# Kernel optimization log

Measured on AMD Instinct MI355X. Metric: run time of the kernel, lower is better.

The kernel has to match this reference:

```python
import jax, jax.numpy as jnp
import numpy as np


def setup_inputs() -> dict:
    key = jax.random.key(0)
    k1, k2, k3, k4, k5 = jax.random.split(key, 5)
    B, Te, Td, H = 16, 256, 128, 512
    return {
        "encoder_out_seq": jax.random.normal(k1, (B, Te, H), dtype=jnp.float32),
        "decoder_out_seq": jax.random.normal(k2, (B, Td, H), dtype=jnp.float32),
        "W_a": jax.random.normal(k3, (H, H), dtype=jnp.float32) * 0.02,
        "U_a": jax.random.normal(k4, (H, H), dtype=jnp.float32) * 0.02,
        "V_a": jax.random.normal(k5, (H, 1), dtype=jnp.float32) * 0.02,
    }


def reference(encoder_out_seq, decoder_out_seq, W_a, U_a, V_a):
    # encoder_out_seq: [B, Te, H], decoder_out_seq: [B, Td, H]
    # Original loops over decoder timesteps via K.rnn; the math per step is
    # independent, so we compute all timesteps at once (same result).
    W_s = jnp.einsum("beh,hk->bek", encoder_out_seq, W_a)      # [B, Te, H]
    U_h = jnp.einsum("bdh,hk->bdk", decoder_out_seq, U_a)      # [B, Td, H]
    # energies: tanh(W_s + U_h) @ V_a -> [B, Td, Te]
    act = jnp.tanh(W_s[:, None, :, :] + U_h[:, :, None, :])     # [B, Td, Te, H]
    e = jnp.einsum("bdeh,h->bde", act, V_a[:, 0])               # [B, Td, Te]
    e = jax.nn.softmax(e, axis=-1)                              # softmax over encoder steps
    # context: sum_e e * enc -> [B, Td, H]
    c = jnp.einsum("bde,beh->bdh", e, encoder_out_seq)
    return (c, e)
```

## Files before the change

kernel.cpp:

```cpp
#include <hip/hip_runtime.h>

#define B_  16
#define TE_ 256
#define TD_ 128
#define H_  512

#define C_TANH 2.88539008177792681472f
#define LOG2E  1.44269504088896340736f

typedef __attribute__((ext_vector_type(8))) short short8v;
typedef __attribute__((ext_vector_type(4))) float floatx4;

__device__ __forceinline__ float wave_sum(float v) {
#pragma unroll
  for (int m = 32; m; m >>= 1) v += __shfl_xor(v, m, 64);
  return v;
}
__device__ __forceinline__ float wave_max(float v) {
#pragma unroll
  for (int m = 32; m; m >>= 1) v = fmaxf(v, __shfl_xor(v, m, 64));
  return v;
}
__device__ __forceinline__ ushort f2bf(float f) {
  unsigned u = __builtin_bit_cast(unsigned, f);
  u += 0x7fffu + ((u >> 16) & 1u);
  return (ushort)(u >> 16);
}
__device__ __forceinline__ float bf2f(ushort u) {
  return __builtin_bit_cast(float, (unsigned)u << 16);
}
__device__ __forceinline__ unsigned pk2(float a, float b) {
  return (unsigned)f2bf(a) | ((unsigned)f2bf(b) << 16);
}

__global__ __launch_bounds__(256) void prep_T(
    const float* __restrict__ enc, const float* __restrict__ Wa,
    const float* __restrict__ Ua, ushort* __restrict__ encT,
    ushort* __restrict__ WaT, ushort* __restrict__ UaT)
{
  __shared__ float tl[32 * 66];
  const int tid = threadIdx.x;
  const int x = blockIdx.x, y = blockIdx.y, z = blockIdx.z;
  const int r = tid >> 3, g = tid & 7;
  const int hh = tid >> 2, tq = tid & 3;

  const float* s;
  ushort* d;
  long dstr;
  int r0, c0;
  if (y < 8) {
    s = enc + (size_t)z * TE_ * H_;
    d = encT + (size_t)z * H_ * TE_;
    dstr = TE_;
    r0 = y * 32; c0 = x * 64;
  } else {
    s = (y == 8) ? Wa : Ua;
    d = (y == 8) ? WaT : UaT;
    dstr = H_;
    r0 = z * 32; c0 = x * 64;
  }

  float4 f0 = *(const float4*)(s + (size_t)(r0 + r) * H_ + c0 + g * 8);
  float4 f1 = *(const float4*)(s + (size_t)(r0 + r) * H_ + c0 + g * 8 + 4);
  float* t = &tl[r * 66 + g * 8];
  t[0] = f0.x; t[1] = f0.y; t[2] = f0.z; t[3] = f0.w;
  t[4] = f1.x; t[5] = f1.y; t[6] = f1.z; t[7] = f1.w;
  __syncthreads();
  float v[8];
#pragma unroll
  for (int i = 0; i < 8; ++i) v[i] = tl[(tq * 8 + i) * 66 + hh];
  uint4 tp = {pk2(v[0], v[1]), pk2(v[2], v[3]), pk2(v[4], v[5]), pk2(v[6], v[7])};
  *(uint4*)(d + (size_t)(c0 + hh) * dstr + r0 + tq * 8) = tp;
}

template <bool CVTA, bool CVTB>
__device__ __forceinline__ void gemm_core(
    const void* Asrc, const void* Bsrc, long lda, long ldb, int K,
    int arow0, int brow0, ushort* As, ushort* Bs, floatx4* acc)
{
  const int tid = threadIdx.x;
  const int l = tid & 63, w = tid >> 6;
  const int l15 = l & 15, l4 = l >> 4;
  const int srow = tid >> 3, kg = tid & 7;
  const int ks = kg >> 2, kc = (kg & 3) << 3;
  const int dsA = ks * 2560 + kc;

  const float*  Af = (const float*)Asrc;
  const ushort* Ab = (const ushort*)Asrc;
  const float*  Bf = (const float*)Bsrc;
  const ushort* Bb = (const ushort*)Bsrc;

  const long aoff0 = (long)(arow0 + srow) * lda + kg * 8;
  const long aoff1 = (long)(arow0 + 32 + srow) * lda + kg * 8;
  const long boff0 = (long)(brow0 + srow) * ldb + kg * 8;
  const long boff1 = (long)(brow0 + 32 + srow) * ldb + kg * 8;

  short8v a0r, a1r, b0r, b1r;
  float4 fa00, fa01, fa10, fa11, fb00, fb01, fb10, fb11;

  auto LD = [&](int kt) {
    if constexpr (CVTA) {
      fa00 = *(const float4*)(Af + aoff0 + kt);
      fa01 = *(const float4*)(Af + aoff0 + kt + 4);
      fa10 = *(const float4*)(Af + aoff1 + kt);
      fa11 = *(const float4*)(Af + aoff1 + kt + 4);
    } else {
      a0r = *(const short8v*)(Ab + aoff0 + kt);
      a1r = *(const short8v*)(Ab + aoff1 + kt);
    }
    if constexpr (CVTB) {
      fb00 = *(const float4*)(Bf + boff0 + kt);
      fb01 = *(const float4*)(Bf + boff0 + kt + 4);
      fb10 = *(const float4*)(Bf + boff1 + kt);
      fb11 = *(const float4*)(Bf + boff1 + kt + 4);
    } else {
      b0r = *(const short8v*)(Bb + boff0 + kt);
      b1r = *(const short8v*)(Bb + boff1 + kt);
    }
  };
  auto ST = [&]() {
    if constexpr (CVTA) {
      uint4 p0 = {pk2(fa00.x, fa00.y), pk2(fa00.z, fa00.w),
                  pk2(fa01.x, fa01.y), pk2(fa01.z, fa01.w)};
      uint4 p1 = {pk2(fa10.x, fa10.y), pk2(fa10.z, fa10.w),
                  pk2(fa11.x, fa11.y), pk2(fa11.z, fa11.w)};
      *(uint4*)&As[dsA + srow * 40] = p0;
      *(uint4*)&As[dsA + (32 + srow) * 40] = p1;
    } else {
      *(short8v*)&As[dsA + srow * 40] = a0r;
      *(short8v*)&As[dsA + (32 + srow) * 40] = a1r;
    }
    if constexpr (CVTB) {
      uint4 p0 = {pk2(fb00.x, fb00.y), pk2(fb00.z, fb00.w),
                  pk2(fb01.x, fb01.y), pk2(fb01.z, fb01.w)};
      uint4 p1 = {pk2(fb10.x, fb10.y), pk2(fb10.z, fb10.w),
                  pk2(fb11.x, fb11.y), pk2(fb11.z, fb11.w)};
      *(uint4*)&Bs[dsA + srow * 40] = p0;
      *(uint4*)&Bs[dsA + (32 + srow) * 40] = p1;
    } else {
      *(short8v*)&Bs[dsA + srow * 40] = b0r;
      *(short8v*)&Bs[dsA + (32 + srow) * 40] = b1r;
    }
  };

  LD(0);
  for (int kt = 0; kt < K; kt += 64) {
    if (kt) __syncthreads();
    ST();
    __syncthreads();
    if (kt + 64 < K) LD(kt + 64);
#pragma unroll
    for (int kk = 0; kk < 2; ++kk) {
      short8v av = *(short8v*)&As[kk * 2560 + (w * 16 + l15) * 40 + l4 * 8];
#pragma unroll
      for (int nt = 0; nt < 4; ++nt) {
        short8v bv = *(short8v*)&Bs[kk * 2560 + (nt * 16 + l15) * 40 + l4 * 8];
        acc[nt] = __builtin_amdgcn_mfma_f32_16x16x32_bf16(av, bv, acc[nt], 0, 0, 0);
      }
    }
  }
}

__global__ __launch_bounds__(256) void gemm_phaseA(
    const float* __restrict__ enc, const ushort* __restrict__ WaT,
    ushort* __restrict__ E_T,
    const float* __restrict__ dec, const ushort* __restrict__ UaT,
    float* __restrict__ eU)
{
  __shared__ __attribute__((aligned(16))) ushort As[5120];
  __shared__ __attribute__((aligned(16))) ushort Bs[5120];

  const int tid = threadIdx.x;
  const int l = tid & 63, w = tid >> 6;
  const int l15 = l & 15, l4 = l >> 4;
  const int id = blockIdx.x;

  floatx4 acc[4] = {};

  if (id < 512) {
    const int x = id & 7, k = id >> 3;
    const int bm = k >> 3;
    const int bn = x * 8 + (k & 7);
    gemm_core<false, true>(WaT, enc, H_, H_, H_, bm * 64, bn * 64, As, Bs, acc);
    const int bb = bn >> 2, t0 = (bn & 3) * 64;
    const int hb = bm * 64 + w * 16 + (l4 << 2);
#pragma unroll
    for (int nt = 0; nt < 4; ++nt) {
      const int t = t0 + nt * 16 + l15;
#pragma unroll
      for (int r = 0; r < 4; ++r)
        E_T[((size_t)bb * H_ + hb + r) * TE_ + t] =
            f2bf(__builtin_amdgcn_exp2f(C_TANH * acc[nt][r]));
    }
  } else {
    const int i2 = id - 512;
    const int x = i2 & 7, k = i2 >> 3;
    const int bm = x * 4 + (k & 3);
    const int bn = k >> 2;
    gemm_core<true, false>(dec, UaT, H_, H_, H_, bm * 64, bn * 64, As, Bs, acc);
    const int growb = bm * 64 + w * 16 + (l4 << 2);
#pragma unroll
    for (int nt = 0; nt < 4; ++nt) {
      const int gcol = bn * 64 + nt * 16 + l15;
#pragma unroll
      for (int r = 0; r < 4; ++r)
        eU[(size_t)(growb + r) * H_ + gcol] =
            __builtin_amdgcn_exp2f(C_TANH * acc[nt][r]);
    }
  }
}

__global__ __launch_bounds__(256) void gemm_ctx(
    const ushort* __restrict__ eB, const ushort* __restrict__ encT,
    float* __restrict__ C)
{
  __shared__ __attribute__((aligned(16))) ushort As[5120];
  __shared__ __attribute__((aligned(16))) ushort Bs[5120];

  const int tid = threadIdx.x;
  const int l = tid & 63, w = tid >> 6;
  const int l15 = l & 15, l4 = l >> 4;
  const long z = blockIdx.z;
  const int bm = blockIdx.y, bn = blockIdx.x;

  floatx4 acc[4] = {};
  gemm_core<false, false>(eB + z * TD_ * TE_, encT + z * (long)H_ * TE_,
                          TE_, TE_, TE_, bm * 64, bn * 64, As, Bs, acc);

  const int growb = bm * 64 + w * 16 + (l4 << 2);
#pragma unroll
  for (int nt = 0; nt < 4; ++nt) {
    const int gcol = bn * 64 + nt * 16 + l15;
#pragma unroll
    for (int r = 0; r < 4; ++r)
      C[(z * TD_ + growb + r) * (long)H_ + gcol] = acc[nt][r];
  }
}

__global__ __launch_bounds__(512) void energies_softmax(
    const ushort* __restrict__ E_T, const float* __restrict__ eU,
    const float* __restrict__ Va, float* __restrict__ e_out,
    ushort* __restrict__ eB)
{
  __shared__ float part[2][8][TE_];

  const int tid  = threadIdx.x;
  const int lane = tid & 63;
  const int wv   = __builtin_amdgcn_readfirstlane(tid >> 6);
  const int id   = blockIdx.x;
  const int xcd  = id & 7, j = id >> 3;
  const int b    = (xcd << 1) | (j >> 6);
  const int d0   = (j & 63) << 1;

  float4 v0 = *(const float4*)(Va + (lane << 2));
  float4 v1 = *(const float4*)(Va + 256 + (lane << 2));
  const float svtot =
      wave_sum(v0.x + v0.y + v0.z + v0.w + v1.x + v1.y + v1.z + v1.w);

  const float* u0 = eU + (size_t)(b * TD_ + d0 + 0) * H_ + wv * 64;
  const float* u1 = eU + (size_t)(b * TD_ + d0 + 1) * H_ + wv * 64;
  const float* vp = Va + wv * 64;
  const ushort* ep = E_T + ((size_t)(b * H_) + wv * 64) * TE_ + (lane << 2);

  float p0[4] = {}, p1[4] = {};

#pragma unroll 4
  for (int h = 0; h < 64; ++h) {
    const float sV = vp[h];
    const float sU0 = u0[h], sU1 = u1[h];
    ushort4 ew = *(const ushort4*)(ep + (size_t)h * TE_);
    float e0 = bf2f(ew.x), e1 = bf2f(ew.y), e2 = bf2f(ew.z), e3 = bf2f(ew.w);
    p0[0] = fmaf(sV, __builtin_amdgcn_rcpf(fmaf(e0, sU0, 1.f)), p0[0]);
    p0[1] = fmaf(sV, __builtin_amdgcn_rcpf(fmaf(e1, sU0, 1.f)), p0[1]);
    p0[2] = fmaf(sV, __builtin_amdgcn_rcpf(fmaf(e2, sU0, 1.f)), p0[2]);
    p0[3] = fmaf(sV, __builtin_amdgcn_rcpf(fmaf(e3, sU0, 1.f)), p0[3]);
    p1[0] = fmaf(sV, __builtin_amdgcn_rcpf(fmaf(e0, sU1, 1.f)), p1[0]);
    p1[1] = fmaf(sV, __builtin_amdgcn_rcpf(fmaf(e1, sU1, 1.f)), p1[1]);
    p1[2] = fmaf(sV, __builtin_amdgcn_rcpf(fmaf(e2, sU1, 1.f)), p1[2]);
    p1[3] = fmaf(sV, __builtin_amdgcn_rcpf(fmaf(e3, sU1, 1.f)), p1[3]);
  }

  *(float4*)&part[0][wv][lane << 2] = *(float4*)p0;
  *(float4*)&part[1][wv][lane << 2] = *(float4*)p1;
  __syncthreads();

  if (wv < 2) {
    float l4v[4] = {0.f, 0.f, 0.f, 0.f};
#pragma unroll
    for (int w = 0; w < 8; ++w) {
      float4 q = *(const float4*)&part[wv][w][lane << 2];
      l4v[0] += q.x; l4v[1] += q.y; l4v[2] += q.z; l4v[3] += q.w;
    }
#pragma unroll
    for (int q = 0; q < 4; ++q) l4v[q] = svtot - 2.f * l4v[q];
    float m = wave_max(fmaxf(fmaxf(l4v[0], l4v[1]), fmaxf(l4v[2], l4v[3])));
    float p[4];
    float s = 0.f;
#pragma unroll
    for (int q = 0; q < 4; ++q) {
      p[q] = __builtin_amdgcn_exp2f((l4v[q] - m) * LOG2E);
      s += p[q];
    }
    s = wave_sum(s);
    const float inv = 1.0f / s;
    float4 ov = {p[0] * inv, p[1] * inv, p[2] * inv, p[3] * inv};
    const size_t ro = (size_t)(b * TD_ + d0 + wv) * TE_ + (lane << 2);
    *(float4*)(e_out + ro) = ov;
    ushort4 ob = {f2bf(ov.x), f2bf(ov.y), f2bf(ov.z), f2bf(ov.w)};
    *(ushort4*)(eB + ro) = ob;
  }
}

extern "C" void kernel_launch(void* const* d_in, const int* in_sizes, int n_in,
                              void* d_out, int out_size, void* d_ws, size_t ws_size,
                              hipStream_t stream) {
  const float* enc = (const float*)d_in[0];
  const float* dec = (const float*)d_in[1];
  const float* Wa  = (const float*)d_in[2];
  const float* Ua  = (const float*)d_in[3];
  const float* Va  = (const float*)d_in[4];

  float* out_c = (float*)d_out;
  float* out_e = out_c + (size_t)B_ * TD_ * H_;

  char* w8 = (char*)d_ws;
  ushort* E_T  = (ushort*)(w8);
  float*  eU   = (float*)(w8 + (4u << 20));
  ushort* WaT  = (ushort*)(w8 + (8u << 20));
  ushort* UaT  = (ushort*)(w8 + (8u << 20) + (512u << 10));
  ushort* encT = (ushort*)(w8 + (9u << 20));
  ushort* eB   = (ushort*)(w8 + (13u << 20));

  prep_T<<<dim3(8, 10, 16), 256, 0, stream>>>(enc, Wa, Ua, encT, WaT, UaT);

  gemm_phaseA<<<768, 256, 0, stream>>>(enc, WaT, E_T, dec, UaT, eU);

  energies_softmax<<<1024, 512, 0, stream>>>(E_T, eU, Va, out_e, eB);

  gemm_ctx<<<dim3(8, 2, 16), 256, 0, stream>>>(eB, encT, out_c);
}
```

Measured before the change: 58.65 us.

## Remove transpose prep kernel by transposing fp32 operands inside GEMM tile loads

Drops the separate prep_T kernel that transposed and converted enc, W_a and U_a to bf16. The GEMM core gains a third load mode that reads row-major fp32 K-major tiles and transposes them into shared memory while packing to bf16. This removes one kernel launch and a full read and write pass over enc and the weights. In exchange each GEMM does scalar 32-bit LDS stores, which may cause bank conflicts, and re-reads fp32 data, doubling global traffic for those operands.

Result: no change. 58.52 us (-0.2%).

```diff
diff --git a/kernel.cpp b/kernel.cpp
--- a/kernel.cpp
+++ b/kernel.cpp
@@ -33,47 +33,7 @@
   return (unsigned)f2bf(a) | ((unsigned)f2bf(b) << 16);
 }
 
-__global__ __launch_bounds__(256) void prep_T(
-    const float* __restrict__ enc, const float* __restrict__ Wa,
-    const float* __restrict__ Ua, ushort* __restrict__ encT,
-    ushort* __restrict__ WaT, ushort* __restrict__ UaT)
-{
-  __shared__ float tl[32 * 66];
-  const int tid = threadIdx.x;
-  const int x = blockIdx.x, y = blockIdx.y, z = blockIdx.z;
-  const int r = tid >> 3, g = tid & 7;
-  const int hh = tid >> 2, tq = tid & 3;
-
-  const float* s;
-  ushort* d;
-  long dstr;
-  int r0, c0;
-  if (y < 8) {
-    s = enc + (size_t)z * TE_ * H_;
-    d = encT + (size_t)z * H_ * TE_;
-    dstr = TE_;
-    r0 = y * 32; c0 = x * 64;
-  } else {
-    s = (y == 8) ? Wa : Ua;
-    d = (y == 8) ? WaT : UaT;
-    dstr = H_;
-    r0 = z * 32; c0 = x * 64;
-  }
-
-  float4 f0 = *(const float4*)(s + (size_t)(r0 + r) * H_ + c0 + g * 8);
-  float4 f1 = *(const float4*)(s + (size_t)(r0 + r) * H_ + c0 + g * 8 + 4);
-  float* t = &tl[r * 66 + g * 8];
-  t[0] = f0.x; t[1] = f0.y; t[2] = f0.z; t[3] = f0.w;
-  t[4] = f1.x; t[5] = f1.y; t[6] = f1.z; t[7] = f1.w;
-  __syncthreads();
-  float v[8];
-#pragma unroll
-  for (int i = 0; i < 8; ++i) v[i] = tl[(tq * 8 + i) * 66 + hh];
-  uint4 tp = {pk2(v[0], v[1]), pk2(v[2], v[3]), pk2(v[4], v[5]), pk2(v[6], v[7])};
-  *(uint4*)(d + (size_t)(c0 + hh) * dstr + r0 + tq * 8) = tp;
-}
-
-template <bool CVTA, bool CVTB>
+template <int MA, int MB>
 __device__ __forceinline__ void gemm_core(
     const void* Asrc, const void* Bsrc, long lda, long ldb, int K,
     int arow0, int brow0, ushort* As, ushort* Bs, floatx4* acc)
@@ -82,8 +42,9 @@
   const int l = tid & 63, w = tid >> 6;
   const int l15 = l & 15, l4 = l >> 4;
   const int srow = tid >> 3, kg = tid & 7;
-  const int ks = kg >> 2, kc = (kg & 3) << 3;
-  const int dsA = ks * 2560 + kc;
+  const int dsRC = (kg >> 2) * 2560 + ((kg & 3) << 3);
+  const int kp = tid >> 3, hg = tid & 7;
+  const int dsT = (kp >> 4) * 2560 + ((kp << 1) & 31);
 
   const float*  Af = (const float*)Asrc;
   const ushort* Ab = (const ushort*)Asrc;
@@ -96,50 +57,82 @@
   const long boff1 = (long)(brow0 + 32 + srow) * ldb + kg * 8;
 
   short8v a0r, a1r, b0r, b1r;
-  float4 fa00, fa01, fa10, fa11, fb00, fb01, fb10, fb11;
+  float4 fa0, fa1, fa2, fa3, fb0, fb1, fb2, fb3;
 
   auto LD = [&](int kt) {
-    if constexpr (CVTA) {
-      fa00 = *(const float4*)(Af + aoff0 + kt);
-      fa01 = *(const float4*)(Af + aoff0 + kt + 4);
-      fa10 = *(const float4*)(Af + aoff1 + kt);
-      fa11 = *(const float4*)(Af + aoff1 + kt + 4);
-    } else {
+    if constexpr (MA == 0) {
       a0r = *(const short8v*)(Ab + aoff0 + kt);
       a1r = *(const short8v*)(Ab + aoff1 + kt);
-    }
-    if constexpr (CVTB) {
-      fb00 = *(const float4*)(Bf + boff0 + kt);
-      fb01 = *(const float4*)(Bf + boff0 + kt + 4);
-      fb10 = *(const float4*)(Bf + boff1 + kt);
-      fb11 = *(const float4*)(Bf + boff1 + kt + 4);
+    } else if constexpr (MA == 1) {
+      fa0 = *(const float4*)(Af + aoff0 + kt);
+      fa1 = *(const float4*)(Af + aoff0 + kt + 4);
+      fa2 = *(const float4*)(Af + aoff1 + kt);
+      fa3 = *(const float4*)(Af + aoff1 + kt + 4);
     } else {
+      const long base = (long)(kt + 2 * kp) * lda + arow0 + hg * 8;
+      fa0 = *(const float4*)(Af + base);
+      fa1 = *(const float4*)(Af + base + 4);
+      fa2 = *(const float4*)(Af + base + lda);
+      fa3 = *(const float4*)(Af + base + lda + 4);
+    }
+    if constexpr (MB == 0) {
       b0r = *(const short8v*)(Bb + boff0 + kt);
       b1r = *(const short8v*)(Bb + boff1 + kt);
+    } else if constexpr (MB == 1) {
+      fb0 = *(const float4*)(Bf + boff0 + kt);
+      fb1 = *(const float4*)(Bf + boff0 + kt + 4);
+      fb2 = *(const float4*)(Bf + boff1 + kt);
+      fb3 = *(const float4*)(Bf + boff1 + kt + 4);
+    } else {
+      const long base = (long)(kt + 2 * kp) * ldb + brow0 + hg * 8;
+      fb0 = *(const float4*)(Bf + base);
+      fb1 = *(const float4*)(Bf + base + 4);
+      fb2 = *(const float4*)(Bf + base + ldb);
+      fb3 = *(const float4*)(Bf + base + ldb + 4);
     }
   };
   auto ST = [&]() {
-    if constexpr (CVTA) {
-      uint4 p0 = {pk2(fa00.x, fa00.y), pk2(fa00.z, fa00.w),
-                  pk2(fa01.x, fa01.y), pk2(fa01.z, fa01.w)};
-      uint4 p1 = {pk2(fa10.x, fa10.y), pk2(fa10.z, fa10.w),
-                  pk2(fa11.x, fa11.y), pk2(fa11.z, fa11.w)};
-      *(uint4*)&As[dsA + srow * 40] = p0;
-      *(uint4*)&As[dsA + (32 + srow) * 40] = p1;
+    if constexpr (MA == 0) {
+      *(short8v*)&As[dsRC + srow * 40] = a0r;
+      *(short8v*)&As[dsRC + (32 + srow) * 40] = a1r;
+    } else if constexpr (MA == 1) {
+      uint4 p0 = {pk2(fa0.x, fa0.y), pk2(fa0.z, fa0.w),
+                  pk2(fa1.x, fa1.y), pk2(fa1.z, fa1.w)};
+      uint4 p1 = {pk2(fa2.x, fa2.y), pk2(fa2.z, fa2.w),
+                  pk2(fa3.x, fa3.y), pk2(fa3.z, fa3.w)};
+      *(uint4*)&As[dsRC + srow * 40] = p0;
+      *(uint4*)&As[dsRC + (32 + srow) * 40] = p1;
     } else {
-      *(short8v*)&As[dsA + srow * 40] = a0r;
-      *(short8v*)&As[dsA + (32 + srow) * 40] = a1r;
-    }
-    if constexpr (CVTB) {
-      uint4 p0 = {pk2(fb00.x, fb00.y), pk2(fb00.z, fb00.w),
-                  pk2(fb01.x, fb01.y), pk2(fb01.z, fb01.w)};
-      uint4 p1 = {pk2(fb10.x, fb10.y), pk2(fb10.z, fb10.w),
-                  pk2(fb11.x, fb11.y), pk2(fb11.z, fb11.w)};
-      *(uint4*)&Bs[dsA + srow * 40] = p0;
-      *(uint4*)&Bs[dsA + (32 + srow) * 40] = p1;
+      const int h0 = hg * 8;
+      *(unsigned*)&As[dsT + (h0 + 0) * 40] = pk2(fa0.x, fa2.x);
+      *(unsigned*)&As[dsT + (h0 + 1) * 40] = pk2(fa0.y, fa2.y);
+      *(unsigned*)&As[dsT + (h0 + 2) * 40] = pk2(fa0.z, fa2.z);
+      *(unsigned*)&As[dsT + (h0 + 3) * 40] = pk2(fa0.w, fa2.w);
+      *(unsigned*)&As[dsT + (h0 + 4) * 40] = pk2(fa1.x, fa3.x);
+      *(unsigned*)&As[dsT + (h0 + 5) * 40] = pk2(fa1.y, fa3.y);
+      *(unsigned*)&As[dsT + (h0 + 6) * 40] = pk2(fa1.z, fa3.z);
+      *(unsigned*)&As[dsT + (h0 + 7) * 40] = pk2(fa1.w, fa3.w);
+    }
+    if constexpr (MB == 0) {
+      *(short8v*)&Bs[dsRC + srow * 40] = b0r;
+      *(short8v*)&Bs[dsRC + (32 + srow) * 40] = b1r;
+    } else if constexpr (MB == 1) {
+      uint4 p0 = {pk2(fb0.x, fb0.y), pk2(fb0.z, fb0.w),
+                  pk2(fb1.x, fb1.y), pk2(fb1.z, fb1.w)};
+      uint4 p1 = {pk2(fb2.x, fb2.y), pk2(fb2.z, fb2.w),
+                  pk2(fb3.x, fb3.y), pk2(fb3.z, fb3.w)};
+      *(uint4*)&Bs[dsRC + srow * 40] = p0;
+      *(uint4*)&Bs[dsRC + (32 + srow) * 40] = p1;
     } else {
-      *(short8v*)&Bs[dsA + srow * 40] = b0r;
-      *(short8v*)&Bs[dsA + (32 + srow) * 40] = b1r;
+      const int h0 = hg * 8;
+      *(unsigned*)&Bs[dsT + (h0 + 0) * 40] = pk2(fb0.x, fb2.x);
+      *(unsigned*)&Bs[dsT + (h0 + 1) * 40] = pk2(fb0.y, fb2.y);
+      *(unsigned*)&Bs[dsT + (h0 + 2) * 40] = pk2(fb0.z, fb2.z);
+      *(unsigned*)&Bs[dsT + (h0 + 3) * 40] = pk2(fb0.w, fb2.w);
+      *(unsigned*)&Bs[dsT + (h0 + 4) * 40] = pk2(fb1.x, fb3.x);
+      *(unsigned*)&Bs[dsT + (h0 + 5) * 40] = pk2(fb1.y, fb3.y);
+      *(unsigned*)&Bs[dsT + (h0 + 6) * 40] = pk2(fb1.z, fb3.z);
+      *(unsigned*)&Bs[dsT + (h0 + 7) * 40] = pk2(fb1.w, fb3.w);
     }
   };
 
@@ -162,9 +155,9 @@
 }
 
 __global__ __launch_bounds__(256) void gemm_phaseA(
-    const float* __restrict__ enc, const ushort* __restrict__ WaT,
+    const float* __restrict__ enc, const float* __restrict__ Wa,
     ushort* __restrict__ E_T,
-    const float* __restrict__ dec, const ushort* __restrict__ UaT,
+    const float* __restrict__ dec, const float* __restrict__ Ua,
     float* __restrict__ eU)
 {
   __shared__ __attribute__((aligned(16))) ushort As[5120];
@@ -181,7 +174,7 @@
     const int x = id & 7, k = id >> 3;
     const int bm = k >> 3;
     const int bn = x * 8 + (k & 7);
-    gemm_core<false, true>(WaT, enc, H_, H_, H_, bm * 64, bn * 64, As, Bs, acc);
+    gemm_core<2, 1>(Wa, enc, H_, H_, H_, bm * 64, bn * 64, As, Bs, acc);
     const int bb = bn >> 2, t0 = (bn & 3) * 64;
     const int hb = bm * 64 + w * 16 + (l4 << 2);
 #pragma unroll
@@ -197,7 +190,7 @@
     const int x = i2 & 7, k = i2 >> 3;
     const int bm = x * 4 + (k & 3);
     const int bn = k >> 2;
-    gemm_core<true, false>(dec, UaT, H_, H_, H_, bm * 64, bn * 64, As, Bs, acc);
+    gemm_core<1, 2>(dec, Ua, H_, H_, H_, bm * 64, bn * 64, As, Bs, acc);
     const int growb = bm * 64 + w * 16 + (l4 << 2);
 #pragma unroll
     for (int nt = 0; nt < 4; ++nt) {
@@ -211,7 +204,7 @@
 }
 
 __global__ __launch_bounds__(256) void gemm_ctx(
-    const ushort* __restrict__ eB, const ushort* __restrict__ encT,
+    const ushort* __restrict__ eB, const float* __restrict__ enc,
     float* __restrict__ C)
 {
   __shared__ __attribute__((aligned(16))) ushort As[5120];
@@ -224,8 +217,8 @@
   const int bm = blockIdx.y, bn = blockIdx.x;
 
   floatx4 acc[4] = {};
-  gemm_core<false, false>(eB + z * TD_ * TE_, encT + z * (long)H_ * TE_,
-                          TE_, TE_, TE_, bm * 64, bn * 64, As, Bs, acc);
+  gemm_core<0, 2>(eB + z * TD_ * TE_, enc + z * (long)TE_ * H_,
+                  TE_, H_, TE_, bm * 64, bn * 64, As, Bs, acc);
 
   const int growb = bm * 64 + w * 16 + (l4 << 2);
 #pragma unroll
@@ -324,18 +317,13 @@
   float* out_e = out_c + (size_t)B_ * TD_ * H_;
 
   char* w8 = (char*)d_ws;
-  ushort* E_T  = (ushort*)(w8);
-  float*  eU   = (float*)(w8 + (4u << 20));
-  ushort* WaT  = (ushort*)(w8 + (8u << 20));
-  ushort* UaT  = (ushort*)(w8 + (8u << 20) + (512u << 10));
-  ushort* encT = (ushort*)(w8 + (9u << 20));
-  ushort* eB   = (ushort*)(w8 + (13u << 20));
-
-  prep_T<<<dim3(8, 10, 16), 256, 0, stream>>>(enc, Wa, Ua, encT, WaT, UaT);
-
-  gemm_phaseA<<<768, 256, 0, stream>>>(enc, WaT, E_T, dec, UaT, eU);
+  ushort* E_T = (ushort*)(w8);
+  float*  eU  = (float*)(w8 + (4u << 20));
+  ushort* eB  = (ushort*)(w8 + (8u << 20));
+
+  gemm_phaseA<<<768, 256, 0, stream>>>(enc, Wa, E_T, dec, Ua, eU);
 
   energies_softmax<<<1024, 512, 0, stream>>>(E_T, eU, Va, out_e, eB);
 
-  gemm_ctx<<<dim3(8, 2, 16), 256, 0, stream>>>(eB, encT, out_c);
-}
+  gemm_ctx<<<dim3(8, 2, 16), 256, 0, stream>>>(eB, enc, out_c);
+}
```
